# Kernel optimization log

Hardware: AMD Instinct MI355X
Metric: run time of the kernel (lower is better)

Reference implementation:

```python
import jax, jax.numpy as jnp
import numpy as np
from jax import lax

EPS = 1e-5
GROUPS = 8
TDVD_RANGE = 10
SCALE = 1.0
SCALE_FACTOR = 0.5


def setup_inputs() -> dict:
    key = jax.random.key(0)
    k1, k2 = jax.random.split(key)
    x = jax.random.normal(k1, (2, 16, 64, 128, 128), dtype=jnp.float32)
    gn_weight = jnp.ones((16,), dtype=jnp.float32)
    gn_bias = jnp.zeros((16,), dtype=jnp.float32)
    threshold = jnp.ones((1,), dtype=jnp.float32)  # torch fills with 1.0
    conv_weight = jax.random.normal(k2, (16, 16, 3, 3, 3), dtype=jnp.float32) * 0.05
    return {"x": x, "gn_weight": gn_weight, "gn_bias": gn_bias,
            "threshold": threshold, "conv_weight": conv_weight}


def _group_norm(x, w, b):
    B, C, D, H, W = x.shape
    xr = x.reshape(B, GROUPS, C // GROUPS, D, H, W)
    mean = xr.mean(axis=(2, 3, 4, 5), keepdims=True)
    var = xr.var(axis=(2, 3, 4, 5), keepdims=True)
    xn = ((xr - mean) * lax.rsqrt(var + EPS)).reshape(B, C, D, H, W)
    return xn * w.reshape(1, C, 1, 1, 1) + b.reshape(1, C, 1, 1, 1)


def _tdvd_histogram(x):
    # reverseint(x * scale * scale_factor) counted into 21 bins [-10..10], as %.
    y = x * (SCALE * SCALE_FACTOR)
    v = jnp.ceil(y * (y >= 0)) + jnp.floor(y * (y <= 0))
    idx = (v + TDVD_RANGE).astype(jnp.int32)
    valid = (idx >= 0) & (idx <= 2 * TDVD_RANGE)
    hist = jnp.zeros((2 * TDVD_RANGE + 1,), jnp.float32).at[
        jnp.clip(idx, 0, 2 * TDVD_RANGE)].add(jnp.where(valid, 1.0, 0.0))
    return hist / x.size * 100.0


def _threshold_func(x, threshold):
    thr = (threshold[0] + 0.0) / SCALE  # zero_point=0, scale=1.0
    t = jnp.transpose(x, (2, 0, 1, 3, 4))  # [D,B,C,H,W]
    front, back = t[:-1], t[1:]
    d = (back - front) / thr
    d = jnp.where(jnp.abs(d) > 1.0, d, 0.0)  # Hardshrink(1.0)
    d = d * lax.stop_gradient(thr)           # .item() detaches in torch
    out = jnp.concatenate([t[:1], front + d], axis=0)
    return jnp.transpose(out, (1, 2, 0, 3, 4))


def reference(x, gn_weight, gn_bias, threshold, conv_weight):
    x = jax.nn.relu(_group_norm(x, gn_weight, gn_bias))
    hist = _tdvd_histogram(x)
    x = _threshold_func(x, threshold)
    out = lax.conv_general_dilated(
        x, conv_weight, window_strides=(1, 1, 1),
        padding=((1, 1), (1, 1), (1, 1)),
        dimension_numbers=("NCDHW", "OIDHW", "NCDHW"))
    return out, hist
```

## Files before the change

kernel.cpp:

```cpp
#include <hip/hip_runtime.h>

typedef __attribute__((ext_vector_type(8))) short short8;
typedef __attribute__((ext_vector_type(4))) float f32x4;

#define GROUP_ELEMS 2097152
#define NBLK 64

__device__ inline short f2bf(float f) {
  unsigned u = __builtin_bit_cast(unsigned, f);
  unsigned r = (u + 0x7FFFu + ((u >> 16) & 1u)) >> 16;
  return (short)r;
}

__global__ __launch_bounds__(256) void k1_partials(const float* __restrict__ x,
                                                   float2* __restrict__ partials) {
  int group = blockIdx.x >> 6;
  int blk = blockIdx.x & 63;
  const float4* p = (const float4*)(x + (size_t)group * GROUP_ELEMS + (size_t)blk * 32768);
  float sum = 0.f, sq = 0.f;
  for (int i = threadIdx.x; i < 8192; i += 256) {
    float4 v = p[i];
    sum += v.x + v.y + v.z + v.w;
    sq  += v.x*v.x + v.y*v.y + v.z*v.z + v.w*v.w;
  }
  for (int off = 32; off; off >>= 1) {
    sum += __shfl_down(sum, off, 64);
    sq  += __shfl_down(sq,  off, 64);
  }
  __shared__ float2 sw[4];
  int lane = threadIdx.x & 63, wid = threadIdx.x >> 6;
  if (lane == 0) sw[wid] = make_float2(sum, sq);
  __syncthreads();
  if (threadIdx.x == 0) {
    float s = 0.f, q = 0.f;
    for (int j = 0; j < 4; ++j) { s += sw[j].x; q += sw[j].y; }
    partials[blockIdx.x] = make_float2(s, q);
  }
}

__global__ void k2_stats(const float2* __restrict__ partials,
                         float2* __restrict__ stats, int* __restrict__ hist) {
  int t = threadIdx.x;
  if (t < 16) {
    float s = 0.f, q = 0.f;
    for (int j = 0; j < NBLK; ++j) { float2 p = partials[t * NBLK + j]; s += p.x; q += p.y; }
    float mean = s / (float)GROUP_ELEMS;
    float var  = q / (float)GROUP_ELEMS - mean * mean;
    stats[t] = make_float2(mean, rsqrtf(var + 1e-5f));
  }
  if (t < 21) hist[t] = 0;
}

__global__ void k2b_wprep(const float* __restrict__ wgt, unsigned short* __restrict__ fbw) {
  int t = threadIdx.x;
  int cc = t >> 6, lane = t & 63;
  int m = lane & 15, g = lane >> 4;
  int icb = (g & 1) * 8, g2 = g >> 1;
  int kpos = 2 * cc + g2;
  short8 f;
  #pragma unroll
  for (int j = 0; j < 8; ++j)
    f[j] = (kpos <= 26) ? f2bf(wgt[m * 432 + (icb + j) * 27 + kpos]) : (short)0;
  *(short8*)(fbw + t * 8) = f;
}

__global__ __launch_bounds__(256) void k3_norm_thresh_hist(
    const float* __restrict__ x, const float* __restrict__ gw, const float* __restrict__ gb,
    const float* __restrict__ thrp, const float2* __restrict__ stats,
    unsigned short* __restrict__ z, int* __restrict__ hist) {
  __shared__ int sh[21];
  int t = threadIdx.x;
  if (t < 21) sh[t] = 0;
  __syncthreads();
  int hwl = t & 31, cp = t >> 5;
  int b = blockIdx.x >> 9;
  int hw = (blockIdx.x & 511) * 32 + hwl;
  int c0 = cp * 2, c1 = c0 + 1;
  float2 st = stats[b * 8 + cp];
  float A0 = gw[c0] * st.y, B0 = gb[c0] - st.x * A0;
  float A1 = gw[c1] * st.y, B1 = gb[c1] - st.x * A1;
  float thr = thrp[0];
  const float* px0 = x + (size_t)(b * 16 + c0) * 1048576 + hw;
  const float* px1 = x + (size_t)(b * 16 + c1) * 1048576 + hw;
  unsigned* pz = (unsigned*)(z + ((size_t)b * 64 * 16384 + hw) * 16 + c0);
  int c10 = 0, c11 = 0, c12 = 0;
  float xv0 = px0[0], xv1 = px1[0];
  float yp0 = 0.f, yp1 = 0.f;
  for (int d = 0; d < 64; ++d) {
    float n0 = 0.f, n1 = 0.f;
    if (d < 63) { n0 = px0[(d + 1) * 16384]; n1 = px1[(d + 1) * 16384]; }
    float y0 = fmaxf(fmaf(xv0, A0, B0), 0.f);
    float y1 = fmaxf(fmaf(xv1, A1, B1), 0.f);
    float v0 = ceilf(0.5f * y0);
    if (v0 == 0.f) c10++; else if (v0 == 1.f) c11++; else if (v0 == 2.f) c12++;
    else if (v0 <= 10.f) atomicAdd(&sh[(int)v0 + 10], 1);
    float v1 = ceilf(0.5f * y1);
    if (v1 == 0.f) c10++; else if (v1 == 1.f) c11++; else if (v1 == 2.f) c12++;
    else if (v1 <= 10.f) atomicAdd(&sh[(int)v1 + 10], 1);
    float z0, z1;
    if (d == 0) { z0 = y0; z1 = y1; }
    else {
      float dd0 = (y0 - yp0) / thr;
      z0 = (fabsf(dd0) > 1.f) ? fmaf(dd0, thr, yp0) : yp0;
      float dd1 = (y1 - yp1) / thr;
      z1 = (fabsf(dd1) > 1.f) ? fmaf(dd1, thr, yp1) : yp1;
    }
    unsigned u = (unsigned)(unsigned short)f2bf(z0) | ((unsigned)(unsigned short)f2bf(z1) << 16);
    pz[d * 131072] = u;
    yp0 = y0; yp1 = y1;
    xv0 = n0; xv1 = n1;
  }
  atomicAdd(&sh[10], c10);
  atomicAdd(&sh[11], c11);
  atomicAdd(&sh[12], c12);
  __syncthreads();
  if (t < 21) atomicAdd(&hist[t], sh[t]);
}

#define DT 4
__global__ __launch_bounds__(256, 3) void k4_conv(const unsigned short* __restrict__ z,
                                                  const unsigned short* __restrict__ fbw,
                                                  float* __restrict__ out) {
  __shared__ unsigned short lz[4 * 10 * 34 * 16];
  const int t = threadIdx.x;
  const int lane = t & 63, wid = t >> 6;
  const int b = blockIdx.z;
  const int d0 = blockIdx.y * DT;
  const int h0 = (blockIdx.x >> 2) * 8, w0 = (blockIdx.x & 3) * 32;
  const int m = lane & 15, g = lane >> 4;
  const int icb = (g & 1) * 8;

  short8 fb[14];
  #pragma unroll
  for (int cc = 0; cc < 14; ++cc)
    fb[cc] = *(const short8*)(fbw + (cc * 64 + lane) * 8);

  const unsigned short* zb = z + (size_t)b * 64 * 16384 * 16;

  for (int gi = t; gi < 2040; gi += 256) {
    int ap = gi / 680;
    int r2 = gi - ap * 680;
    int r = r2 / 68;
    int rem = r2 - r * 68;
    int s = rem >> 1, ig = rem & 1;
    int dg = d0 - 1 + ap, hg = h0 - 1 + r, wg = w0 - 1 + s;
    short8 v = {0,0,0,0,0,0,0,0};
    if ((unsigned)dg < 64u && (unsigned)hg < 128u && (unsigned)wg < 128u)
      v = *(const short8*)(zb + ((size_t)dg * 16384 + hg * 128 + wg) * 16 + ig * 8);
    *(short8*)(&lz[((ap * 10 + r) * 34 + s) * 16 + ig * 8]) = v;
  }
  __syncthreads();

  #pragma unroll
  for (int dl = 0; dl < DT; ++dl) {
    short8 sv0 = {0,0,0,0,0,0,0,0}, sv1 = {0,0,0,0,0,0,0,0}, sv2 = {0,0,0,0,0,0,0,0};
    int so0 = 0, so1 = 0, so2 = -1;
    if (dl < DT - 1) {
      const int ap = dl + 3, sl = ap & 3;
      const int dg = d0 - 1 + ap;
      {
        int gi = t;
        int r = gi / 68, rem = gi - r * 68, s = rem >> 1, ig = rem & 1;
        int hg = h0 - 1 + r, wg = w0 - 1 + s;
        so0 = ((sl * 10 + r) * 34 + s) * 16 + ig * 8;
        if ((unsigned)dg < 64u && (unsigned)hg < 128u && (unsigned)wg < 128u)
          sv0 = *(const short8*)(zb + ((size_t)dg * 16384 + hg * 128 + wg) * 16 + ig * 8);
      }
      {
        int gi = t + 256;
        int r = gi / 68, rem = gi - r * 68, s = rem >> 1, ig = rem & 1;
        int hg = h0 - 1 + r, wg = w0 - 1 + s;
        so1 = ((sl * 10 + r) * 34 + s) * 16 + ig * 8;
        if ((unsigned)dg < 64u && (unsigned)hg < 128u && (unsigned)wg < 128u)
          sv1 = *(const short8*)(zb + ((size_t)dg * 16384 + hg * 128 + wg) * 16 + ig * 8);
      }
      if (t < 168) {
        int gi = t + 512;
        int r = gi / 68, rem = gi - r * 68, s = rem >> 1, ig = rem & 1;
        int hg = h0 - 1 + r, wg = w0 - 1 + s;
        so2 = ((sl * 10 + r) * 34 + s) * 16 + ig * 8;
        if ((unsigned)dg < 64u && (unsigned)hg < 128u && (unsigned)wg < 128u)
          sv2 = *(const short8*)(zb + ((size_t)dg * 16384 + hg * 128 + wg) * 16 + ig * 8);
      }
    }
    #pragma unroll
    for (int q = 0; q < 4; ++q) {
      const int hl = wid * 2 + (q >> 1), wt = q & 1;
      const int lb = (hl * 34 + wt * 16 + m) * 16 + icb;
      f32x4 acc = {0.f, 0.f, 0.f, 0.f};
      __builtin_amdgcn_s_setprio(1);
      #pragma unroll
      for (int cc = 0; cc < 14; ++cc) {
        const int kp0 = 2 * cc;
        const int kp1 = (2 * cc + 1 > 26) ? 26 : 2 * cc + 1;
        const int o0 = ((((dl + kp0 / 9) & 3) * 10 + (kp0 % 9) / 3) * 34 + (kp0 % 3)) * 16;
        const int o1 = ((((dl + kp1 / 9) & 3) * 10 + (kp1 % 9) / 3) * 34 + (kp1 % 3)) * 16;
        int off = lb + (g >= 2 ? o1 : o0);
        short8 a = *(const short8*)(&lz[off]);
        acc = __builtin_amdgcn_mfma_f32_16x16x32_bf16(a, fb[cc], acc, 0, 0, 0);
      }
      __builtin_amdgcn_s_setprio(0);
      float* op = out + (((size_t)(b * 16 + m) * 64 + (d0 + dl)) * 128 + (h0 + hl)) * 128
                  + w0 + wt * 16 + g * 4;
      *(float4*)op = make_float4(acc[0], acc[1], acc[2], acc[3]);
    }
    if (dl < DT - 1) {
      *(short8*)(&lz[so0]) = sv0;
      *(short8*)(&lz[so1]) = sv1;
      if (so2 >= 0) *(short8*)(&lz[so2]) = sv2;
      __syncthreads();
    }
  }
}

__global__ void k5_hist_out(const int* __restrict__ hist, float* __restrict__ out) {
  int t = threadIdx.x;
  if (t < 21) out[33554432u + t] = (float)hist[t] * (100.0f / 33554432.0f);
}

extern "C" void kernel_launch(void* const* d_in, const int* in_sizes, int n_in,
                              void* d_out, int out_size, void* d_ws, size_t ws_size,
                              hipStream_t stream) {
  (void)in_sizes; (void)n_in; (void)out_size; (void)ws_size;
  const float* x   = (const float*)d_in[0];
  const float* gw  = (const float*)d_in[1];
  const float* gb  = (const float*)d_in[2];
  const float* thr = (const float*)d_in[3];
  const float* cw  = (const float*)d_in[4];
  float* out = (float*)d_out;

  char* ws = (char*)d_ws;
  unsigned short* z = (unsigned short*)ws;
  float2* partials = (float2*)(ws + (size_t)67108864);
  float2* stats    = (float2*)(ws + (size_t)67108864 + 8192);
  int*    hist     = (int*)  (ws + (size_t)67108864 + 8192 + 128);
  unsigned short* fbw = (unsigned short*)(ws + (size_t)67108864 + 16384);

  k1_partials<<<1024, 256, 0, stream>>>(x, partials);
  k2_stats<<<1, 64, 0, stream>>>(partials, stats, hist);
  k2b_wprep<<<1, 896, 0, stream>>>(cw, fbw);
  k3_norm_thresh_hist<<<1024, 256, 0, stream>>>(x, gw, gb, thr, stats, z, hist);
  k4_conv<<<dim3(64, 16, 2), 256, 0, stream>>>(z, fbw, out);
  k5_hist_out<<<1, 64, 0, stream>>>(hist, out);
}
```

Before: 150.5 us.

## Stream depth planes into LDS via direct global-to-LDS loads with rolling accumulators

```diff
diff --git a/kernel.cpp b/kernel.cpp
--- a/kernel.cpp
+++ b/kernel.cpp
@@ -10,6 +10,12 @@
   unsigned u = __builtin_bit_cast(unsigned, f);
   unsigned r = (u + 0x7FFFu + ((u >> 16) & 1u)) >> 16;
   return (short)r;
+}
+
+__device__ inline void gload_lds16(const void* g, void* l) {
+  __builtin_amdgcn_global_load_lds(
+      (const __attribute__((address_space(1))) unsigned int*)g,
+      (__attribute__((address_space(3))) unsigned int*)l, 16, 0, 0);
 }
 
 __global__ __launch_bounds__(256) void k1_partials(const float* __restrict__ x,
@@ -51,17 +57,22 @@
   if (t < 21) hist[t] = 0;
 }
 
-__global__ void k2b_wprep(const float* __restrict__ wgt, unsigned short* __restrict__ fbw) {
-  int t = threadIdx.x;
-  int cc = t >> 6, lane = t & 63;
-  int m = lane & 15, g = lane >> 4;
-  int icb = (g & 1) * 8, g2 = g >> 1;
-  int kpos = 2 * cc + g2;
-  short8 f;
-  #pragma unroll
-  for (int j = 0; j < 8; ++j)
-    f[j] = (kpos <= 26) ? f2bf(wgt[m * 432 + (icb + j) * 27 + kpos]) : (short)0;
-  *(short8*)(fbw + t * 8) = f;
+__global__ void k2b_wprep(const float* __restrict__ wgt, unsigned short* __restrict__ fbw2,
+                          unsigned int* __restrict__ dummy) {
+  int t = threadIdx.x;
+  if (t < 960) {
+    int f = t >> 6, lane = t & 63;
+    int kd = f / 5, c = f - kd * 5;
+    int m = lane & 15, g = lane >> 4;
+    int icb = (g & 1) * 8, g2 = g >> 1;
+    int tap = 2 * c + g2;
+    short8 v;
+    #pragma unroll
+    for (int j = 0; j < 8; ++j)
+      v[j] = (tap <= 8) ? f2bf(wgt[m * 432 + (icb + j) * 27 + kd * 9 + tap]) : (short)0;
+    *(short8*)(fbw2 + t * 8) = v;
+  }
+  if (t >= 960 && t < 976) dummy[t - 960] = 0;
 }
 
 __global__ __launch_bounds__(256) void k3_norm_thresh_hist(
@@ -72,42 +83,50 @@
   int t = threadIdx.x;
   if (t < 21) sh[t] = 0;
   __syncthreads();
-  int hwl = t & 31, cp = t >> 5;
-  int b = blockIdx.x >> 9;
-  int hw = (blockIdx.x & 511) * 32 + hwl;
+  int bx = blockIdx.x;
+  int b = bx >> 9, cp = (bx >> 6) & 7, part = (bx >> 2) & 15, dchunk = bx & 3;
+  int hw = (part * 256 + t) * 4;
   int c0 = cp * 2, c1 = c0 + 1;
   float2 st = stats[b * 8 + cp];
   float A0 = gw[c0] * st.y, B0 = gb[c0] - st.x * A0;
   float A1 = gw[c1] * st.y, B1 = gb[c1] - st.x * A1;
   float thr = thrp[0];
-  const float* px0 = x + (size_t)(b * 16 + c0) * 1048576 + hw;
-  const float* px1 = x + (size_t)(b * 16 + c1) * 1048576 + hw;
-  unsigned* pz = (unsigned*)(z + ((size_t)b * 64 * 16384 + hw) * 16 + c0);
+  const f32x4* px0 = (const f32x4*)(x + (size_t)(b * 16 + c0) * 1048576 + hw);
+  const f32x4* px1 = (const f32x4*)(x + (size_t)(b * 16 + c1) * 1048576 + hw);
+  unsigned* pz = (unsigned*)(z + ((size_t)b * 1048576 + hw) * 16 + c0);
   int c10 = 0, c11 = 0, c12 = 0;
-  float xv0 = px0[0], xv1 = px1[0];
-  float yp0 = 0.f, yp1 = 0.f;
-  for (int d = 0; d < 64; ++d) {
-    float n0 = 0.f, n1 = 0.f;
-    if (d < 63) { n0 = px0[(d + 1) * 16384]; n1 = px1[(d + 1) * 16384]; }
-    float y0 = fmaxf(fmaf(xv0, A0, B0), 0.f);
-    float y1 = fmaxf(fmaf(xv1, A1, B1), 0.f);
-    float v0 = ceilf(0.5f * y0);
-    if (v0 == 0.f) c10++; else if (v0 == 1.f) c11++; else if (v0 == 2.f) c12++;
-    else if (v0 <= 10.f) atomicAdd(&sh[(int)v0 + 10], 1);
-    float v1 = ceilf(0.5f * y1);
-    if (v1 == 0.f) c10++; else if (v1 == 1.f) c11++; else if (v1 == 2.f) c12++;
-    else if (v1 <= 10.f) atomicAdd(&sh[(int)v1 + 10], 1);
-    float z0, z1;
-    if (d == 0) { z0 = y0; z1 = y1; }
-    else {
-      float dd0 = (y0 - yp0) / thr;
-      z0 = (fabsf(dd0) > 1.f) ? fmaf(dd0, thr, yp0) : yp0;
-      float dd1 = (y1 - yp1) / thr;
-      z1 = (fabsf(dd1) > 1.f) ? fmaf(dd1, thr, yp1) : yp1;
+  const int lo = dchunk * 16, dend = lo + 16;
+  const int dstart = (lo == 0) ? 0 : lo - 1;
+  f32x4 xv0 = px0[(size_t)dstart * 4096], xv1 = px1[(size_t)dstart * 4096];
+  float yp0[4], yp1[4];
+  for (int d = dstart; d < dend; ++d) {
+    f32x4 n0 = {0.f,0.f,0.f,0.f}, n1 = {0.f,0.f,0.f,0.f};
+    if (d + 1 < dend) { n0 = px0[(size_t)(d + 1) * 4096]; n1 = px1[(size_t)(d + 1) * 4096]; }
+    bool act = (d >= lo);
+    #pragma unroll
+    for (int k = 0; k < 4; ++k) {
+      float y0 = fmaxf(fmaf(xv0[k], A0, B0), 0.f);
+      float y1 = fmaxf(fmaf(xv1[k], A1, B1), 0.f);
+      if (act) {
+        float v0 = ceilf(0.5f * y0);
+        if (v0 == 0.f) c10++; else if (v0 == 1.f) c11++; else if (v0 == 2.f) c12++;
+        else if (v0 <= 10.f) atomicAdd(&sh[(int)v0 + 10], 1);
+        float v1 = ceilf(0.5f * y1);
+        if (v1 == 0.f) c10++; else if (v1 == 1.f) c11++; else if (v1 == 2.f) c12++;
+        else if (v1 <= 10.f) atomicAdd(&sh[(int)v1 + 10], 1);
+        float z0, z1;
+        if (d == 0) { z0 = y0; z1 = y1; }
+        else {
+          float dd0 = (y0 - yp0[k]) / thr;
+          z0 = (fabsf(dd0) > 1.f) ? fmaf(dd0, thr, yp0[k]) : yp0[k];
+          float dd1 = (y1 - yp1[k]) / thr;
+          z1 = (fabsf(dd1) > 1.f) ? fmaf(dd1, thr, yp1[k]) : yp1[k];
+        }
+        unsigned u = (unsigned)(unsigned short)f2bf(z0) | ((unsigned)(unsigned short)f2bf(z1) << 16);
+        pz[d * 131072 + k * 8] = u;
+      }
+      yp0[k] = y0; yp1[k] = y1;
     }
-    unsigned u = (unsigned)(unsigned short)f2bf(z0) | ((unsigned)(unsigned short)f2bf(z1) << 16);
-    pz[d * 131072] = u;
-    yp0 = y0; yp1 = y1;
     xv0 = n0; xv1 = n1;
   }
   atomicAdd(&sh[10], c10);
@@ -117,100 +136,124 @@
   if (t < 21) atomicAdd(&hist[t], sh[t]);
 }
 
-#define DT 4
-__global__ __launch_bounds__(256, 3) void k4_conv(const unsigned short* __restrict__ z,
-                                                  const unsigned short* __restrict__ fbw,
+#define DT 8
+#define PLANE 5440
+__global__ __launch_bounds__(256, 4) void k4_conv(const unsigned short* __restrict__ z,
+                                                  const unsigned short* __restrict__ fbw2,
+                                                  const char* __restrict__ dummyc,
                                                   float* __restrict__ out) {
-  __shared__ unsigned short lz[4 * 10 * 34 * 16];
+  __shared__ unsigned short lz[2 * PLANE];
   const int t = threadIdx.x;
   const int lane = t & 63, wid = t >> 6;
   const int b = blockIdx.z;
   const int d0 = blockIdx.y * DT;
   const int h0 = (blockIdx.x >> 2) * 8, w0 = (blockIdx.x & 3) * 32;
   const int m = lane & 15, g = lane >> 4;
-  const int icb = (g & 1) * 8;
-
-  short8 fb[14];
+  const int icb = (g & 1) * 8, g2 = g >> 1;
+
+  short8 fb2[15];
   #pragma unroll
-  for (int cc = 0; cc < 14; ++cc)
-    fb[cc] = *(const short8*)(fbw + (cc * 64 + lane) * 8);
-
-  const unsigned short* zb = z + (size_t)b * 64 * 16384 * 16;
-
-  for (int gi = t; gi < 2040; gi += 256) {
-    int ap = gi / 680;
-    int r2 = gi - ap * 680;
-    int r = r2 / 68;
-    int rem = r2 - r * 68;
-    int s = rem >> 1, ig = rem & 1;
-    int dg = d0 - 1 + ap, hg = h0 - 1 + r, wg = w0 - 1 + s;
-    short8 v = {0,0,0,0,0,0,0,0};
-    if ((unsigned)dg < 64u && (unsigned)hg < 128u && (unsigned)wg < 128u)
-      v = *(const short8*)(zb + ((size_t)dg * 16384 + hg * 128 + wg) * 16 + ig * 8);
-    *(short8*)(&lz[((ap * 10 + r) * 34 + s) * 16 + ig * 8]) = v;
-  }
-  __syncthreads();
-
+  for (int f = 0; f < 15; ++f)
+    fb2[f] = *(const short8*)(fbw2 + (f * 64 + lane) * 8);
+
+  int tco[5];
   #pragma unroll
-  for (int dl = 0; dl < DT; ++dl) {
-    short8 sv0 = {0,0,0,0,0,0,0,0}, sv1 = {0,0,0,0,0,0,0,0}, sv2 = {0,0,0,0,0,0,0,0};
-    int so0 = 0, so1 = 0, so2 = -1;
-    if (dl < DT - 1) {
-      const int ap = dl + 3, sl = ap & 3;
-      const int dg = d0 - 1 + ap;
-      {
-        int gi = t;
-        int r = gi / 68, rem = gi - r * 68, s = rem >> 1, ig = rem & 1;
-        int hg = h0 - 1 + r, wg = w0 - 1 + s;
-        so0 = ((sl * 10 + r) * 34 + s) * 16 + ig * 8;
-        if ((unsigned)dg < 64u && (unsigned)hg < 128u && (unsigned)wg < 128u)
-          sv0 = *(const short8*)(zb + ((size_t)dg * 16384 + hg * 128 + wg) * 16 + ig * 8);
-      }
-      {
-        int gi = t + 256;
-        int r = gi / 68, rem = gi - r * 68, s = rem >> 1, ig = rem & 1;
-        int hg = h0 - 1 + r, wg = w0 - 1 + s;
-        so1 = ((sl * 10 + r) * 34 + s) * 16 + ig * 8;
-        if ((unsigned)dg < 64u && (unsigned)hg < 128u && (unsigned)wg < 128u)
-          sv1 = *(const short8*)(zb + ((size_t)dg * 16384 + hg * 128 + wg) * 16 + ig * 8);
-      }
-      if (t < 168) {
-        int gi = t + 512;
-        int r = gi / 68, rem = gi - r * 68, s = rem >> 1, ig = rem & 1;
-        int hg = h0 - 1 + r, wg = w0 - 1 + s;
-        so2 = ((sl * 10 + r) * 34 + s) * 16 + ig * 8;
-        if ((unsigned)dg < 64u && (unsigned)hg < 128u && (unsigned)wg < 128u)
-          sv2 = *(const short8*)(zb + ((size_t)dg * 16384 + hg * 128 + wg) * 16 + ig * 8);
-      }
-    }
-    #pragma unroll
-    for (int q = 0; q < 4; ++q) {
-      const int hl = wid * 2 + (q >> 1), wt = q & 1;
-      const int lb = (hl * 34 + wt * 16 + m) * 16 + icb;
-      f32x4 acc = {0.f, 0.f, 0.f, 0.f};
-      __builtin_amdgcn_s_setprio(1);
-      #pragma unroll
-      for (int cc = 0; cc < 14; ++cc) {
-        const int kp0 = 2 * cc;
-        const int kp1 = (2 * cc + 1 > 26) ? 26 : 2 * cc + 1;
-        const int o0 = ((((dl + kp0 / 9) & 3) * 10 + (kp0 % 9) / 3) * 34 + (kp0 % 3)) * 16;
-        const int o1 = ((((dl + kp1 / 9) & 3) * 10 + (kp1 % 9) / 3) * 34 + (kp1 % 3)) * 16;
-        int off = lb + (g >= 2 ? o1 : o0);
-        short8 a = *(const short8*)(&lz[off]);
-        acc = __builtin_amdgcn_mfma_f32_16x16x32_bf16(a, fb[cc], acc, 0, 0, 0);
-      }
-      __builtin_amdgcn_s_setprio(0);
-      float* op = out + (((size_t)(b * 16 + m) * 64 + (d0 + dl)) * 128 + (h0 + hl)) * 128
-                  + w0 + wt * 16 + g * 4;
-      *(float4*)op = make_float4(acc[0], acc[1], acc[2], acc[3]);
-    }
-    if (dl < DT - 1) {
-      *(short8*)(&lz[so0]) = sv0;
-      *(short8*)(&lz[so1]) = sv1;
-      if (so2 >= 0) *(short8*)(&lz[so2]) = sv2;
-      __syncthreads();
-    }
-  }
+  for (int c = 0; c < 5; ++c) {
+    int tap = 2 * c + g2; if (tap > 8) tap = 8;
+    tco[c] = ((tap / 3) * 34 + (tap % 3)) * 16;
+  }
+
+  const char* zbc = (const char*)(z + (size_t)b * 16777216);
+
+  const int cb0 = wid * 64;
+  const int cb1 = 256 + wid * 64;
+  const int cb2 = (wid == 0) ? 512 : (wid == 1) ? 576 : 616;
+  long long hob0, hob1, hob2; bool hv0, hv1, hv2;
+  {
+    int gi, r, rem, s, ig, hg, wg;
+    gi = cb0 + lane; r = gi / 68; rem = gi - r * 68; s = rem >> 1; ig = rem & 1;
+    hg = h0 - 1 + r; wg = w0 - 1 + s;
+    hv0 = ((unsigned)hg < 128u) && ((unsigned)wg < 128u);
+    hob0 = ((long long)(hg * 128 + wg) * 16 + ig * 8) * 2;
+    gi = cb1 + lane; r = gi / 68; rem = gi - r * 68; s = rem >> 1; ig = rem & 1;
+    hg = h0 - 1 + r; wg = w0 - 1 + s;
+    hv1 = ((unsigned)hg < 128u) && ((unsigned)wg < 128u);
+    hob1 = ((long long)(hg * 128 + wg) * 16 + ig * 8) * 2;
+    gi = cb2 + lane; r = gi / 68; rem = gi - r * 68; s = rem >> 1; ig = rem & 1;
+    hg = h0 - 1 + r; wg = w0 - 1 + s;
+    hv2 = ((unsigned)hg < 128u) && ((unsigned)wg < 128u);
+    hob2 = ((long long)(hg * 128 + wg) * 16 + ig * 8) * 2;
+  }
+
+  const f32x4 fzero = {0.f, 0.f, 0.f, 0.f};
+  f32x4 A0[4], A1[4], A2[4];
+  #pragma unroll
+  for (int q = 0; q < 4; ++q) { A0[q] = fzero; A1[q] = fzero; A2[q] = fzero; }
+
+  {
+    const int dg = d0 - 1;
+    const long long dgo = (long long)dg * 524288;
+    const bool pd = (unsigned)dg < 64u;
+    gload_lds16((pd && hv0) ? zbc + dgo + hob0 : dummyc, &lz[cb0 * 8]);
+    gload_lds16((pd && hv1) ? zbc + dgo + hob1 : dummyc, &lz[cb1 * 8]);
+    if (wid < 3)
+      gload_lds16((pd && hv2) ? zbc + dgo + hob2 : dummyc, &lz[cb2 * 8]);
+  }
+  __syncthreads();
+
+#define BODY(PH, AS, AM, AN, DOJ2, DOJ1, DOJ0, DOLOAD, DOSTORE)                         \
+  {                                                                                     \
+    const int ph_ = (PH);                                                               \
+    if (DOLOAD) {                                                                       \
+      const int dg = d0 + ph_;                                                          \
+      const long long dgo = (long long)dg * 524288;                                     \
+      const bool pd = (unsigned)dg < 64u;                                               \
+      const unsigned sl = ((unsigned)(ph_ + 1) & 1u) * PLANE;                           \
+      gload_lds16((pd && hv0) ? zbc + dgo + hob0 : dummyc, &lz[sl + cb0 * 8]);          \
+      gload_lds16((pd && hv1) ? zbc + dgo + hob1 : dummyc, &lz[sl + cb1 * 8]);          \
+      if (wid < 3)                                                                      \
+        gload_lds16((pd && hv2) ? zbc + dgo + hob2 : dummyc, &lz[sl + cb2 * 8]);        \
+    }                                                                                   \
+    const unsigned su = ((unsigned)ph_ & 1u) * PLANE;                                   \
+    __builtin_amdgcn_s_setprio(1);                                                      \
+    _Pragma("unroll")                                                                   \
+    for (int q = 0; q < 4; ++q) {                                                       \
+      const int hl = wid * 2 + (q >> 1), wt = q & 1;                                    \
+      const int qb = (hl * 34 + wt * 16 + m) * 16 + icb + (int)su;                      \
+      _Pragma("unroll")                                                                 \
+      for (int c = 0; c < 5; ++c) {                                                     \
+        short8 a = *(const short8*)(&lz[qb + tco[c]]);                                  \
+        if (DOJ2) AN[q] = __builtin_amdgcn_mfma_f32_16x16x32_bf16(a, fb2[c], AN[q], 0, 0, 0);      \
+        if (DOJ1) AM[q] = __builtin_amdgcn_mfma_f32_16x16x32_bf16(a, fb2[5 + c], AM[q], 0, 0, 0);  \
+        if (DOJ0) AS[q] = __builtin_amdgcn_mfma_f32_16x16x32_bf16(a, fb2[10 + c], AS[q], 0, 0, 0); \
+      }                                                                                 \
+    }                                                                                   \
+    __builtin_amdgcn_s_setprio(0);                                                      \
+    if (DOSTORE) {                                                                      \
+      const int dd = d0 + ph_ - 2;                                                      \
+      _Pragma("unroll")                                                                 \
+      for (int q = 0; q < 4; ++q) {                                                     \
+        const int hl = wid * 2 + (q >> 1), wt = q & 1;                                  \
+        float* op = out + (((size_t)(b * 16 + m) * 64 + dd) * 128 + (h0 + hl)) * 128    \
+                    + w0 + wt * 16 + g * 4;                                             \
+        *(float4*)op = make_float4(AS[q][0], AS[q][1], AS[q][2], AS[q][3]);             \
+        AS[q] = fzero;                                                                  \
+      }                                                                                 \
+    }                                                                                   \
+    __syncthreads();                                                                    \
+  }
+
+  BODY(0, A1, A2, A0, 1, 0, 0, 1, 0)
+  BODY(1, A2, A0, A1, 1, 1, 0, 1, 0)
+  BODY(2, A0, A1, A2, 1, 1, 1, 1, 1)
+  #pragma unroll 1
+  for (int pp = 3; pp <= 6; pp += 3) {
+    BODY(pp,     A1, A2, A0, 1, 1, 1, 1, 1)
+    BODY(pp + 1, A2, A0, A1, 1, 1, 1, 1, 1)
+    BODY(pp + 2, A0, A1, A2, 1, 1, 1, 1, 1)
+  }
+  BODY(9, A1, A2, A0, 0, 0, 1, 0, 1)
+#undef BODY
 }
 
 __global__ void k5_hist_out(const int* __restrict__ hist, float* __restrict__ out) {
@@ -231,15 +274,16 @@
 
   char* ws = (char*)d_ws;
   unsigned short* z = (unsigned short*)ws;
-  float2* partials = (float2*)(ws + (size_t)67108864);
-  float2* stats    = (float2*)(ws + (size_t)67108864 + 8192);
-  int*    hist     = (int*)  (ws + (size_t)67108864 + 8192 + 128);
-  unsigned short* fbw = (unsigned short*)(ws + (size_t)67108864 + 16384);
+  float2* partials  = (float2*)(ws + (size_t)67108864);
+  float2* stats     = (float2*)(ws + (size_t)67108864 + 8192);
+  int*    hist      = (int*)  (ws + (size_t)67108864 + 8192 + 128);
+  unsigned int* dummy = (unsigned int*)(ws + (size_t)67108864 + 8448);
+  unsigned short* fbw2 = (unsigned short*)(ws + (size_t)67108864 + 16384);
 
   k1_partials<<<1024, 256, 0, stream>>>(x, partials);
   k2_stats<<<1, 64, 0, stream>>>(partials, stats, hist);
-  k2b_wprep<<<1, 896, 0, stream>>>(cw, fbw);
+  k2b_wprep<<<1, 1024, 0, stream>>>(cw, fbw2, dummy);
   k3_norm_thresh_hist<<<1024, 256, 0, stream>>>(x, gw, gb, thr, stats, z, hist);
-  k4_conv<<<dim3(64, 16, 2), 256, 0, stream>>>(z, fbw, out);
+  k4_conv<<<dim3(64, 8, 2), 256, 0, stream>>>(z, fbw2, (const char*)dummy, out);
   k5_hist_out<<<1, 64, 0, stream>>>(hist, out);
 }
```

Measured after the change: 226.4 us. 50.4% more time.
